# Performance work log

Measured on AMD Instinct MI355X. Metric: run time of the kernel, lower is better.

## Reference

```python
import jax, jax.numpy as jnp
import numpy as np

N_EMBED = 1024
HEAD_SIZE = 64
SEQ_LEN = 4096
BATCH = 4


def setup_inputs() -> dict:
    key = jax.random.key(0)
    ks = jax.random.split(key, 7)
    scale = 1.0 / np.sqrt(N_EMBED)
    return {
        "x": jax.random.normal(ks[0], (BATCH, SEQ_LEN, N_EMBED), dtype=jnp.float32),
        "Wq": jax.random.normal(ks[1], (N_EMBED, HEAD_SIZE), dtype=jnp.float32) * scale,
        "bq": jax.random.normal(ks[2], (HEAD_SIZE,), dtype=jnp.float32) * 0.01,
        "Wk": jax.random.normal(ks[3], (N_EMBED, HEAD_SIZE), dtype=jnp.float32) * scale,
        "bk": jax.random.normal(ks[4], (HEAD_SIZE,), dtype=jnp.float32) * 0.01,
        "Wv": jax.random.normal(ks[5], (N_EMBED, HEAD_SIZE), dtype=jnp.float32) * scale,
        "bv": jax.random.normal(ks[6], (HEAD_SIZE,), dtype=jnp.float32) * 0.01,
    }


def reference(x, Wq, bq, Wk, bk, Wv, bv):
    # q, k, v: [B, S, H]
    q = x @ Wq + bq
    k = x @ Wk + bk
    v = x @ Wv + bv
    # raw scores [B, S, S]; original masks to -inf THEN divides by sqrt(head_size)
    # (-inf / sqrt = -inf, so equivalent to scaling finite entries only)
    scores = jnp.einsum("bqh,bkh->bqk", q, k)
    seq_len = x.shape[1]
    causal = jnp.tril(jnp.ones((seq_len, seq_len), dtype=bool))
    inv_scale = 1.0 / jnp.sqrt(jnp.asarray(HEAD_SIZE, dtype=scores.dtype))
    scores = jnp.where(causal, scores * inv_scale, -jnp.inf)
    weight = jax.nn.softmax(scores, axis=-1)
    # dropout is identity in eval / p=0
    out = jnp.einsum("bqk,bkh->bqh", weight, v)
    return out
```

## Files before the change

kernel.cpp:

```cpp
#include <hip/hip_runtime.h>
#include <hip/hip_bf16.h>

#define SS 4096
#define NROW 16384

typedef __attribute__((ext_vector_type(8))) short short8;
typedef __attribute__((ext_vector_type(4))) short short4_t;
typedef __attribute__((ext_vector_type(4))) float f32x4;

static __device__ __forceinline__ short f2bf(float f) {
    union { float f; unsigned u; } v; v.f = f;
    unsigned r = v.u + 0x7FFFu + ((v.u >> 16) & 1u);
    return (short)(r >> 16);
}
static __device__ __forceinline__ float bf2f(short s) {
    union { unsigned u; float f; } v;
    v.u = ((unsigned)(unsigned short)s) << 16;
    return v.f;
}

__global__ __launch_bounds__(256) void pack_w(const float* __restrict__ Wq,
                                              const float* __restrict__ Wk,
                                              const float* __restrict__ Wv,
                                              short* __restrict__ Wpack) {
    int t = blockIdx.x * 256 + threadIdx.x;
    int n = t % 192;
    int k = t / 192;
    const float* W = (n < 64) ? Wq : (n < 128 ? Wk : Wv);
    int nn = n & 63;
    Wpack[n * 1024 + k] = f2bf(W[k * 64 + nn]);
}

__global__ __launch_bounds__(256, 2) void proj_qkv(const float* __restrict__ x,
                                                   const short* __restrict__ Wpack,
                                                   const float* __restrict__ bq,
                                                   const float* __restrict__ bk,
                                                   const float* __restrict__ bv,
                                                   short* __restrict__ Qg,
                                                   short* __restrict__ Kg,
                                                   short* __restrict__ Vt) {
    __shared__ short Xs[2][32 * 72];
    __shared__ short Wsm[2][192 * 72];
    int tid = threadIdx.x, lane = tid & 63, wv = tid >> 6;
    int g = lane >> 4, c = lane & 15;
    int mh = wv & 1, nh = wv >> 1;
    int rowbase = blockIdx.x * 32;

    f32x4 acc[6];
    for (int i = 0; i < 6; ++i) acc[i] = (f32x4)(0.f);

    int xrow0 = tid >> 4, xc = tid & 15;
    const float* xp0 = x + (rowbase + xrow0) * 1024 + xc * 4;
    const float* xp1 = x + (rowbase + 16 + xrow0) * 1024 + xc * 4;

    float4 xr0 = *reinterpret_cast<const float4*>(xp0);
    float4 xr1 = *reinterpret_cast<const float4*>(xp1);
    short8 wr[6];
    for (int j = 0; j < 6; ++j) {
        int u = tid + j * 256;
        wr[j] = *reinterpret_cast<const short8*>(Wpack + (u >> 3) * 1024 + (u & 7) * 8);
    }

    for (int ko = 0; ko < 16; ++ko) {
        int bs = ko & 1;
        short4_t s0, s1;
        s0.x = f2bf(xr0.x); s0.y = f2bf(xr0.y); s0.z = f2bf(xr0.z); s0.w = f2bf(xr0.w);
        s1.x = f2bf(xr1.x); s1.y = f2bf(xr1.y); s1.z = f2bf(xr1.z); s1.w = f2bf(xr1.w);
        *reinterpret_cast<short4_t*>(&Xs[bs][xrow0 * 72 + xc * 4]) = s0;
        *reinterpret_cast<short4_t*>(&Xs[bs][(16 + xrow0) * 72 + xc * 4]) = s1;
        for (int j = 0; j < 6; ++j) {
            int u = tid + j * 256;
            *reinterpret_cast<short8*>(&Wsm[bs][(u >> 3) * 72 + (u & 7) * 8]) = wr[j];
        }
        if (ko < 15) {
            int k0 = (ko + 1) * 64;
            xr0 = *reinterpret_cast<const float4*>(xp0 + k0);
            xr1 = *reinterpret_cast<const float4*>(xp1 + k0);
            for (int j = 0; j < 6; ++j) {
                int u = tid + j * 256;
                wr[j] = *reinterpret_cast<const short8*>(Wpack + (u >> 3) * 1024 + k0 + (u & 7) * 8);
            }
        }
        __syncthreads();
        for (int kc = 0; kc < 2; ++kc) {
            short8 a = *reinterpret_cast<const short8*>(&Xs[bs][(mh * 16 + c) * 72 + kc * 32 + g * 8]);
            for (int nt = 0; nt < 6; ++nt) {
                short8 b = *reinterpret_cast<const short8*>(&Wsm[bs][(nh * 96 + nt * 16 + c) * 72 + kc * 32 + g * 8]);
                acc[nt] = __builtin_amdgcn_mfma_f32_16x16x32_bf16(a, b, acc[nt], 0, 0, 0);
            }
        }
    }

    const float SCQ = 0.125f * 1.4426950408889634f;
    for (int nt = 0; nt < 6; ++nt) {
        int col = nh * 96 + nt * 16 + c;
        for (int r = 0; r < 4; ++r) {
            int grow = rowbase + mh * 16 + g * 4 + r;
            float vv = acc[nt][r];
            if (col < 64) {
                Qg[grow * 64 + col] = f2bf((vv + bq[col]) * SCQ);
            } else if (col < 128) {
                Kg[grow * 64 + (col - 64)] = f2bf(vv + bk[col - 64]);
            } else {
                int f = col - 128;
                int batch = grow >> 12, s = grow & 4095;
                Vt[batch * 262144 + (s >> 6) * 4096 + f * 64 + (s & 63)] = f2bf(vv + bv[f]);
            }
        }
    }
}

__global__ __launch_bounds__(256, 3) void attn(const short* __restrict__ Qg,
                                               const short* __restrict__ Kg,
                                               const short* __restrict__ Vt,
                                               short* __restrict__ Opart,
                                               float* __restrict__ Ls) {
    __shared__ short Kbuf[2][64 * 72];
    __shared__ short Vbuf[2][64 * 72];
    __shared__ short Ps[4][16 * 68];
    int tid = threadIdx.x, lane = tid & 63, wv = tid >> 6;
    int g = lane >> 4, c = lane & 15;

    int b = blockIdx.x;
    int ch = b & 7, P = (b >> 3) & 63, batch = b >> 9;
    int ntall = P + 1;
    int nch = (ntall + 7) >> 3;
    if (ch >= nch) return;
    int t0 = ch * 8, t1 = min(t0 + 8, ntall);

    int qrow0 = batch * SS + P * 64;
    const short* Kb = Kg + batch * SS * 64;
    const short* Vb = Vt + batch * SS * 64;

    short8 aq0 = *reinterpret_cast<const short8*>(Qg + (qrow0 + wv * 16 + c) * 64 + g * 8);
    short8 aq1 = *reinterpret_cast<const short8*>(Qg + (qrow0 + wv * 16 + c) * 64 + 32 + g * 8);

    f32x4 acc_o[4];
    for (int f = 0; f < 4; ++f) acc_o[f] = (f32x4)(0.f);
    float rs[4] = {0.f, 0.f, 0.f, 0.f};

    int u0 = tid, u1 = tid + 256;
    short8 kr0 = *reinterpret_cast<const short8*>(Kb + t0 * 4096 + u0 * 8);
    short8 kr1 = *reinterpret_cast<const short8*>(Kb + t0 * 4096 + u1 * 8);
    short8 vr0 = *reinterpret_cast<const short8*>(Vb + t0 * 4096 + u0 * 8);
    short8 vr1 = *reinterpret_cast<const short8*>(Vb + t0 * 4096 + u1 * 8);

    short* Psw = Ps[wv];

    for (int t = t0; t < t1; ++t) {
        int bs = t & 1;
        *reinterpret_cast<short8*>(&Kbuf[bs][(u0 >> 3) * 72 + (u0 & 7) * 8]) = kr0;
        *reinterpret_cast<short8*>(&Kbuf[bs][(u1 >> 3) * 72 + (u1 & 7) * 8]) = kr1;
        *reinterpret_cast<short8*>(&Vbuf[bs][(u0 >> 3) * 72 + (u0 & 7) * 8]) = vr0;
        *reinterpret_cast<short8*>(&Vbuf[bs][(u1 >> 3) * 72 + (u1 & 7) * 8]) = vr1;
        if (t + 1 < t1) {
            kr0 = *reinterpret_cast<const short8*>(Kb + (t + 1) * 4096 + u0 * 8);
            kr1 = *reinterpret_cast<const short8*>(Kb + (t + 1) * 4096 + u1 * 8);
            vr0 = *reinterpret_cast<const short8*>(Vb + (t + 1) * 4096 + u0 * 8);
            vr1 = *reinterpret_cast<const short8*>(Vb + (t + 1) * 4096 + u1 * 8);
        }
        __syncthreads();

        f32x4 s[4];
        for (int nt = 0; nt < 4; ++nt) s[nt] = (f32x4)(0.f);
        for (int nt = 0; nt < 4; ++nt) {
            short8 b0 = *reinterpret_cast<const short8*>(&Kbuf[bs][(nt * 16 + c) * 72 + g * 8]);
            s[nt] = __builtin_amdgcn_mfma_f32_16x16x32_bf16(aq0, b0, s[nt], 0, 0, 0);
            short8 b1 = *reinterpret_cast<const short8*>(&Kbuf[bs][(nt * 16 + c) * 72 + 32 + g * 8]);
            s[nt] = __builtin_amdgcn_mfma_f32_16x16x32_bf16(aq1, b1, s[nt], 0, 0, 0);
        }

        if (t == P) {
            for (int nt = 0; nt < 4; ++nt)
                for (int r = 0; r < 4; ++r) {
                    int key = nt * 16 + c;
                    int row = wv * 16 + g * 4 + r;
                    float p = (key <= row) ? exp2f(s[nt][r]) : 0.f;
                    rs[r] += p;
                    Psw[(g * 4 + r) * 68 + nt * 16 + c] = f2bf(p);
                }
        } else {
            for (int nt = 0; nt < 4; ++nt)
                for (int r = 0; r < 4; ++r) {
                    float p = exp2f(s[nt][r]);
                    rs[r] += p;
                    Psw[(g * 4 + r) * 68 + nt * 16 + c] = f2bf(p);
                }
        }

        for (int kc2 = 0; kc2 < 2; ++kc2) {
            short8 ap = *reinterpret_cast<const short8*>(&Psw[c * 68 + kc2 * 32 + g * 8]);
            for (int f = 0; f < 4; ++f) {
                short8 bv_ = *reinterpret_cast<const short8*>(&Vbuf[bs][(f * 16 + c) * 72 + kc2 * 32 + g * 8]);
                acc_o[f] = __builtin_amdgcn_mfma_f32_16x16x32_bf16(ap, bv_, acc_o[f], 0, 0, 0);
            }
        }
    }

    float l[4];
    for (int r = 0; r < 4; ++r) {
        float ss = rs[r];
        ss += __shfl_xor(ss, 1);
        ss += __shfl_xor(ss, 2);
        ss += __shfl_xor(ss, 4);
        ss += __shfl_xor(ss, 8);
        l[r] = ss;
    }

    int slot = ((batch * 64 + P) << 3) + ch;
    short* op = Opart + slot * 4096;
    for (int r = 0; r < 4; ++r) {
        float inv = 1.0f / l[r];
        int row = wv * 16 + g * 4 + r;
        for (int f = 0; f < 4; ++f)
            op[row * 64 + f * 16 + c] = f2bf(acc_o[f][r] * inv);
    }
    if (c == 0)
        for (int r = 0; r < 4; ++r)
            Ls[slot * 64 + wv * 16 + g * 4 + r] = l[r];
}

__global__ __launch_bounds__(256) void merge_k(const short* __restrict__ Opart,
                                               const float* __restrict__ Ls,
                                               float* __restrict__ out) {
    int bP = blockIdx.x;
    int P = bP & 63, batch = bP >> 6;
    int nch = (P + 8) >> 3;
    int tid = threadIdx.x;
    int row = tid & 63, fg = tid >> 6;
    int slot0 = bP << 3;

    float w[8];
    float wsum = 0.f;
    for (int i = 0; i < nch; ++i) { w[i] = Ls[(slot0 + i) * 64 + row]; wsum += w[i]; }
    float invw = 1.0f / wsum;

    float o[16];
    for (int j = 0; j < 16; ++j) o[j] = 0.f;
    for (int i = 0; i < nch; ++i) {
        const short* op = Opart + (slot0 + i) * 4096 + row * 64 + fg * 16;
        short8 v0 = *reinterpret_cast<const short8*>(op);
        short8 v1 = *reinterpret_cast<const short8*>(op + 8);
        for (int j = 0; j < 8; ++j) {
            o[j]     += w[i] * bf2f(v0[j]);
            o[8 + j] += w[i] * bf2f(v1[j]);
        }
    }
    int orow = batch * SS + P * 64 + row;
    for (int j = 0; j < 16; j += 4) {
        float4 v;
        v.x = o[j] * invw; v.y = o[j + 1] * invw; v.z = o[j + 2] * invw; v.w = o[j + 3] * invw;
        *reinterpret_cast<float4*>(out + orow * 64 + fg * 16 + j) = v;
    }
}

extern "C" void kernel_launch(void* const* d_in, const int* in_sizes, int n_in,
                              void* d_out, int out_size, void* d_ws, size_t ws_size,
                              hipStream_t stream) {
    const float* x  = (const float*)d_in[0];
    const float* Wq = (const float*)d_in[1];
    const float* bq = (const float*)d_in[2];
    const float* Wk = (const float*)d_in[3];
    const float* bk = (const float*)d_in[4];
    const float* Wv = (const float*)d_in[5];
    const float* bv = (const float*)d_in[6];
    float* out = (float*)d_out;

    short* Wpack = (short*)d_ws;
    short* Qg    = Wpack + 196608;
    short* Kg    = Qg + NROW * 64;
    short* Vt    = Kg + NROW * 64;
    short* Opart = Vt + NROW * 64;
    float* Ls    = (float*)(Opart + 2048 * 4096);

    hipLaunchKernelGGL(pack_w,   dim3(768),  dim3(256), 0, stream, Wq, Wk, Wv, Wpack);
    hipLaunchKernelGGL(proj_qkv, dim3(512),  dim3(256), 0, stream, x, Wpack, bq, bk, bv, Qg, Kg, Vt);
    hipLaunchKernelGGL(attn,     dim3(2048), dim3(256), 0, stream, Qg, Kg, Vt, Opart, Ls);
    hipLaunchKernelGGL(merge_k,  dim3(256),  dim3(256), 0, stream, Opart, Ls, out);
}
```

Before: 178.8 us.

## Use direct global-to-LDS loads with XOR swizzle, compact attention grid, faster bf16/exp

Replaces register-staged global loads in the projection and attention kernels with global_load_lds transfers into XOR-swizzled, unpadded LDS tiles. x is now kept as fp32 in LDS and converted to bf16 at fragment-read time. The attention grid is remapped so that only valid (query tile, chunk) pairs are launched, which removes the empty blocks that previously returned early. It also switches to the hardware exp2 and a cheaper round-to-nearest bf16 conversion, and rewrites pack_w as an LDS-tiled transpose. The risks are subtle swizzle and index bugs, a slightly different rounding mode, and larger fp32 LDS usage.

```diff
diff --git a/kernel.cpp b/kernel.cpp
--- a/kernel.cpp
+++ b/kernel.cpp
@@ -5,14 +5,27 @@
 #define NROW 16384
 
 typedef __attribute__((ext_vector_type(8))) short short8;
-typedef __attribute__((ext_vector_type(4))) short short4_t;
 typedef __attribute__((ext_vector_type(4))) float f32x4;
 
+#define AS1 __attribute__((address_space(1)))
+#define AS3 __attribute__((address_space(3)))
+
+static __device__ __forceinline__ void glds16(const void* g, void* l) {
+    __builtin_amdgcn_global_load_lds((const AS1 unsigned*)g, (AS3 unsigned*)l, 16, 0, 0);
+}
 static __device__ __forceinline__ short f2bf(float f) {
     union { float f; unsigned u; } v; v.f = f;
     unsigned r = v.u + 0x7FFFu + ((v.u >> 16) & 1u);
     return (short)(r >> 16);
 }
+static __device__ __forceinline__ short f2bf_fast(float f) {
+    union { float f; unsigned u; } v; v.f = f;
+    return (short)((v.u + 0x8000u) >> 16);
+}
+static __device__ __forceinline__ unsigned pkbf(float lo, float hi) {
+    union { float f; unsigned u; } x, y; x.f = lo; y.f = hi;
+    return __builtin_amdgcn_perm(y.u + 0x8000u, x.u + 0x8000u, 0x07060302);
+}
 static __device__ __forceinline__ float bf2f(short s) {
     union { unsigned u; float f; } v;
     v.u = ((unsigned)(unsigned short)s) << 16;
@@ -23,12 +36,23 @@
                                               const float* __restrict__ Wk,
                                               const float* __restrict__ Wv,
                                               short* __restrict__ Wpack) {
-    int t = blockIdx.x * 256 + threadIdx.x;
-    int n = t % 192;
-    int k = t / 192;
-    const float* W = (n < 64) ? Wq : (n < 128 ? Wk : Wv);
-    int nn = n & 63;
-    Wpack[n * 1024 + k] = f2bf(W[k * 64 + nn]);
+    __shared__ float T[64 * 65];
+    int bid = blockIdx.x;
+    int nb = bid >> 4, kb = bid & 15;
+    const float* W = (nb == 0) ? Wq : (nb == 1 ? Wk : Wv);
+    int n0 = nb * 64, k0 = kb * 64;
+    int tid = threadIdx.x;
+    for (int ps = 0; ps < 16; ++ps) {
+        int idx = tid + ps * 256;
+        int kk = idx >> 6, nn = idx & 63;
+        T[kk * 65 + nn] = W[(k0 + kk) * 64 + nn];
+    }
+    __syncthreads();
+    for (int ps = 0; ps < 16; ++ps) {
+        int idx = tid + ps * 256;
+        int nn = idx >> 6, kk = idx & 63;
+        Wpack[(n0 + nn) * 1024 + k0 + kk] = f2bf(T[kk * 65 + nn]);
+    }
 }
 
 __global__ __launch_bounds__(256, 2) void proj_qkv(const float* __restrict__ x,
@@ -39,8 +63,8 @@
                                                    short* __restrict__ Qg,
                                                    short* __restrict__ Kg,
                                                    short* __restrict__ Vt) {
-    __shared__ short Xs[2][32 * 72];
-    __shared__ short Wsm[2][192 * 72];
+    __shared__ float Xs[2][32 * 64];
+    __shared__ short Wsm[2][192 * 64];
     int tid = threadIdx.x, lane = tid & 63, wv = tid >> 6;
     int g = lane >> 4, c = lane & 15;
     int mh = wv & 1, nh = wv >> 1;
@@ -49,47 +73,43 @@
     f32x4 acc[6];
     for (int i = 0; i < 6; ++i) acc[i] = (f32x4)(0.f);
 
-    int xrow0 = tid >> 4, xc = tid & 15;
-    const float* xp0 = x + (rowbase + xrow0) * 1024 + xc * 4;
-    const float* xp1 = x + (rowbase + 16 + xrow0) * 1024 + xc * 4;
-
-    float4 xr0 = *reinterpret_cast<const float4*>(xp0);
-    float4 xr1 = *reinterpret_cast<const float4*>(xp1);
-    short8 wr[6];
-    for (int j = 0; j < 6; ++j) {
-        int u = tid + j * 256;
-        wr[j] = *reinterpret_cast<const short8*>(Wpack + (u >> 3) * 1024 + (u & 7) * 8);
-    }
+    int xs0 = (wv * 2 + 0) * 64 + lane, xs1 = (wv * 2 + 1) * 64 + lane;
+    int xr0 = xs0 >> 4, xp0 = (xs0 & 15) ^ (xr0 & 15);
+    int xr1 = xs1 >> 4, xp1 = (xs1 & 15) ^ (xr1 & 15);
+
+#define PROJ_ISSUE(nbs, k0)                                                              \
+    do {                                                                                 \
+        glds16(x + (rowbase + xr0) * 1024 + (k0) + xp0 * 4, &Xs[nbs][(wv * 2 + 0) * 256]); \
+        glds16(x + (rowbase + xr1) * 1024 + (k0) + xp1 * 4, &Xs[nbs][(wv * 2 + 1) * 256]); \
+        for (int j = 0; j < 6; ++j) {                                                    \
+            int ws = (wv * 6 + j) * 64 + lane;                                           \
+            int wr = ws >> 3, wp = (ws & 7) ^ (wr & 7);                                  \
+            glds16(Wpack + wr * 1024 + (k0) + wp * 8, &Wsm[nbs][(wv * 6 + j) * 512]);    \
+        }                                                                                \
+    } while (0)
+
+    PROJ_ISSUE(0, 0);
 
     for (int ko = 0; ko < 16; ++ko) {
         int bs = ko & 1;
-        short4_t s0, s1;
-        s0.x = f2bf(xr0.x); s0.y = f2bf(xr0.y); s0.z = f2bf(xr0.z); s0.w = f2bf(xr0.w);
-        s1.x = f2bf(xr1.x); s1.y = f2bf(xr1.y); s1.z = f2bf(xr1.z); s1.w = f2bf(xr1.w);
-        *reinterpret_cast<short4_t*>(&Xs[bs][xrow0 * 72 + xc * 4]) = s0;
-        *reinterpret_cast<short4_t*>(&Xs[bs][(16 + xrow0) * 72 + xc * 4]) = s1;
-        for (int j = 0; j < 6; ++j) {
-            int u = tid + j * 256;
-            *reinterpret_cast<short8*>(&Wsm[bs][(u >> 3) * 72 + (u & 7) * 8]) = wr[j];
-        }
-        if (ko < 15) {
-            int k0 = (ko + 1) * 64;
-            xr0 = *reinterpret_cast<const float4*>(xp0 + k0);
-            xr1 = *reinterpret_cast<const float4*>(xp1 + k0);
-            for (int j = 0; j < 6; ++j) {
-                int u = tid + j * 256;
-                wr[j] = *reinterpret_cast<const short8*>(Wpack + (u >> 3) * 1024 + k0 + (u & 7) * 8);
-            }
-        }
         __syncthreads();
+        if (ko < 15) PROJ_ISSUE(bs ^ 1, (ko + 1) * 64);
         for (int kc = 0; kc < 2; ++kc) {
-            short8 a = *reinterpret_cast<const short8*>(&Xs[bs][(mh * 16 + c) * 72 + kc * 32 + g * 8]);
+            int h0 = kc * 8 + g * 2;
+            float4 xa = *reinterpret_cast<const float4*>(&Xs[bs][(mh * 16 + c) * 64 + ((h0) ^ c) * 4]);
+            float4 xb = *reinterpret_cast<const float4*>(&Xs[bs][(mh * 16 + c) * 64 + ((h0 + 1) ^ c) * 4]);
+            short8 a;
+            unsigned* aw = (unsigned*)&a;
+            aw[0] = pkbf(xa.x, xa.y); aw[1] = pkbf(xa.z, xa.w);
+            aw[2] = pkbf(xb.x, xb.y); aw[3] = pkbf(xb.z, xb.w);
             for (int nt = 0; nt < 6; ++nt) {
-                short8 b = *reinterpret_cast<const short8*>(&Wsm[bs][(nh * 96 + nt * 16 + c) * 72 + kc * 32 + g * 8]);
+                int wrow = nh * 96 + nt * 16 + c;
+                short8 b = *reinterpret_cast<const short8*>(&Wsm[bs][wrow * 64 + ((g + 4 * kc) ^ (c & 7)) * 8]);
                 acc[nt] = __builtin_amdgcn_mfma_f32_16x16x32_bf16(a, b, acc[nt], 0, 0, 0);
             }
         }
     }
+#undef PROJ_ISSUE
 
     const float SCQ = 0.125f * 1.4426950408889634f;
     for (int nt = 0; nt < 6; ++nt) {
@@ -115,20 +135,26 @@
                                                const short* __restrict__ Vt,
                                                short* __restrict__ Opart,
                                                float* __restrict__ Ls) {
-    __shared__ short Kbuf[2][64 * 72];
-    __shared__ short Vbuf[2][64 * 72];
+    __shared__ short Kbuf[2][64 * 64];
+    __shared__ short Vbuf[2][64 * 64];
     __shared__ short Ps[4][16 * 68];
     int tid = threadIdx.x, lane = tid & 63, wv = tid >> 6;
     int g = lane >> 4, c = lane & 15;
 
-    int b = blockIdx.x;
-    int ch = b & 7, P = (b >> 3) & 63, batch = b >> 9;
-    int ntall = P + 1;
-    int nch = (ntall + 7) >> 3;
-    if (ch >= nch) return;
+    int bid = blockIdx.x;
+    int batch = bid / 288;
+    int j = bid - batch * 288;
+    int gq = (int)((sqrtf((float)j + 1.0f) - 1.0f) * 0.5f);
+    while (4 * (gq + 1) * (gq + 2) <= j) ++gq;
+    while (4 * gq * (gq + 1) > j) --gq;
+    int rem = j - 4 * gq * (gq + 1);
+    int pidx = rem / (gq + 1);
+    int ch = rem - pidx * (gq + 1);
+    int p = gq * 8 + pidx;
+
+    int ntall = p + 1;
     int t0 = ch * 8, t1 = min(t0 + 8, ntall);
-
-    int qrow0 = batch * SS + P * 64;
+    int qrow0 = batch * SS + p * 64;
     const short* Kb = Kg + batch * SS * 64;
     const short* Vb = Vt + batch * SS * 64;
 
@@ -139,63 +165,64 @@
     for (int f = 0; f < 4; ++f) acc_o[f] = (f32x4)(0.f);
     float rs[4] = {0.f, 0.f, 0.f, 0.f};
 
-    int u0 = tid, u1 = tid + 256;
-    short8 kr0 = *reinterpret_cast<const short8*>(Kb + t0 * 4096 + u0 * 8);
-    short8 kr1 = *reinterpret_cast<const short8*>(Kb + t0 * 4096 + u1 * 8);
-    short8 vr0 = *reinterpret_cast<const short8*>(Vb + t0 * 4096 + u0 * 8);
-    short8 vr1 = *reinterpret_cast<const short8*>(Vb + t0 * 4096 + u1 * 8);
-
+    int s0 = (wv * 2 + 0) * 64 + lane, s1 = (wv * 2 + 1) * 64 + lane;
+    int r0 = s0 >> 3, q0 = ((s0 & 7) ^ (r0 & 7));
+    int r1 = s1 >> 3, q1 = ((s1 & 7) ^ (r1 & 7));
+
+#define ATTN_ISSUE(nbs, t)                                                           \
+    do {                                                                             \
+        const short* kt_ = Kb + (t) * 4096;                                          \
+        const short* vt_ = Vb + (t) * 4096;                                          \
+        glds16(kt_ + r0 * 64 + q0 * 8, &Kbuf[nbs][(wv * 2 + 0) * 512]);              \
+        glds16(kt_ + r1 * 64 + q1 * 8, &Kbuf[nbs][(wv * 2 + 1) * 512]);              \
+        glds16(vt_ + r0 * 64 + q0 * 8, &Vbuf[nbs][(wv * 2 + 0) * 512]);              \
+        glds16(vt_ + r1 * 64 + q1 * 8, &Vbuf[nbs][(wv * 2 + 1) * 512]);              \
+    } while (0)
+
+    ATTN_ISSUE(0, t0);
     short* Psw = Ps[wv];
 
     for (int t = t0; t < t1; ++t) {
-        int bs = t & 1;
-        *reinterpret_cast<short8*>(&Kbuf[bs][(u0 >> 3) * 72 + (u0 & 7) * 8]) = kr0;
-        *reinterpret_cast<short8*>(&Kbuf[bs][(u1 >> 3) * 72 + (u1 & 7) * 8]) = kr1;
-        *reinterpret_cast<short8*>(&Vbuf[bs][(u0 >> 3) * 72 + (u0 & 7) * 8]) = vr0;
-        *reinterpret_cast<short8*>(&Vbuf[bs][(u1 >> 3) * 72 + (u1 & 7) * 8]) = vr1;
-        if (t + 1 < t1) {
-            kr0 = *reinterpret_cast<const short8*>(Kb + (t + 1) * 4096 + u0 * 8);
-            kr1 = *reinterpret_cast<const short8*>(Kb + (t + 1) * 4096 + u1 * 8);
-            vr0 = *reinterpret_cast<const short8*>(Vb + (t + 1) * 4096 + u0 * 8);
-            vr1 = *reinterpret_cast<const short8*>(Vb + (t + 1) * 4096 + u1 * 8);
-        }
+        int bs = (t - t0) & 1;
         __syncthreads();
+        if (t + 1 < t1) ATTN_ISSUE(bs ^ 1, t + 1);
 
         f32x4 s[4];
         for (int nt = 0; nt < 4; ++nt) s[nt] = (f32x4)(0.f);
         for (int nt = 0; nt < 4; ++nt) {
-            short8 b0 = *reinterpret_cast<const short8*>(&Kbuf[bs][(nt * 16 + c) * 72 + g * 8]);
+            short8 b0 = *reinterpret_cast<const short8*>(&Kbuf[bs][(nt * 16 + c) * 64 + ((g) ^ (c & 7)) * 8]);
             s[nt] = __builtin_amdgcn_mfma_f32_16x16x32_bf16(aq0, b0, s[nt], 0, 0, 0);
-            short8 b1 = *reinterpret_cast<const short8*>(&Kbuf[bs][(nt * 16 + c) * 72 + 32 + g * 8]);
+            short8 b1 = *reinterpret_cast<const short8*>(&Kbuf[bs][(nt * 16 + c) * 64 + ((g + 4) ^ (c & 7)) * 8]);
             s[nt] = __builtin_amdgcn_mfma_f32_16x16x32_bf16(aq1, b1, s[nt], 0, 0, 0);
         }
 
-        if (t == P) {
+        if (t == p) {
             for (int nt = 0; nt < 4; ++nt)
                 for (int r = 0; r < 4; ++r) {
                     int key = nt * 16 + c;
                     int row = wv * 16 + g * 4 + r;
-                    float p = (key <= row) ? exp2f(s[nt][r]) : 0.f;
-                    rs[r] += p;
-                    Psw[(g * 4 + r) * 68 + nt * 16 + c] = f2bf(p);
+                    float pv = (key <= row) ? __builtin_amdgcn_exp2f(s[nt][r]) : 0.f;
+                    rs[r] += pv;
+                    Psw[(g * 4 + r) * 68 + nt * 16 + c] = f2bf_fast(pv);
                 }
         } else {
             for (int nt = 0; nt < 4; ++nt)
                 for (int r = 0; r < 4; ++r) {
-                    float p = exp2f(s[nt][r]);
-                    rs[r] += p;
-                    Psw[(g * 4 + r) * 68 + nt * 16 + c] = f2bf(p);
+                    float pv = __builtin_amdgcn_exp2f(s[nt][r]);
+                    rs[r] += pv;
+                    Psw[(g * 4 + r) * 68 + nt * 16 + c] = f2bf_fast(pv);
                 }
         }
 
         for (int kc2 = 0; kc2 < 2; ++kc2) {
             short8 ap = *reinterpret_cast<const short8*>(&Psw[c * 68 + kc2 * 32 + g * 8]);
             for (int f = 0; f < 4; ++f) {
-                short8 bv_ = *reinterpret_cast<const short8*>(&Vbuf[bs][(f * 16 + c) * 72 + kc2 * 32 + g * 8]);
+                short8 bv_ = *reinterpret_cast<const short8*>(&Vbuf[bs][(f * 16 + c) * 64 + ((g + 4 * kc2) ^ (c & 7)) * 8]);
                 acc_o[f] = __builtin_amdgcn_mfma_f32_16x16x32_bf16(ap, bv_, acc_o[f], 0, 0, 0);
             }
         }
     }
+#undef ATTN_ISSUE
 
     float l[4];
     for (int r = 0; r < 4; ++r) {
@@ -207,7 +234,7 @@
         l[r] = ss;
     }
 
-    int slot = ((batch * 64 + P) << 3) + ch;
+    int slot = ((batch * 64 + p) << 3) + ch;
     short* op = Opart + slot * 4096;
     for (int r = 0; r < 4; ++r) {
         float inv = 1.0f / l[r];
@@ -236,21 +263,21 @@
     float invw = 1.0f / wsum;
 
     float o[16];
-    for (int j = 0; j < 16; ++j) o[j] = 0.f;
+    for (int jj = 0; jj < 16; ++jj) o[jj] = 0.f;
     for (int i = 0; i < nch; ++i) {
         const short* op = Opart + (slot0 + i) * 4096 + row * 64 + fg * 16;
         short8 v0 = *reinterpret_cast<const short8*>(op);
         short8 v1 = *reinterpret_cast<const short8*>(op + 8);
-        for (int j = 0; j < 8; ++j) {
-            o[j]     += w[i] * bf2f(v0[j]);
-            o[8 + j] += w[i] * bf2f(v1[j]);
+        for (int jj = 0; jj < 8; ++jj) {
+            o[jj]     += w[i] * bf2f(v0[jj]);
+            o[8 + jj] += w[i] * bf2f(v1[jj]);
         }
     }
     int orow = batch * SS + P * 64 + row;
-    for (int j = 0; j < 16; j += 4) {
+    for (int jj = 0; jj < 16; jj += 4) {
         float4 v;
-        v.x = o[j] * invw; v.y = o[j + 1] * invw; v.z = o[j + 2] * invw; v.w = o[j + 3] * invw;
-        *reinterpret_cast<float4*>(out + orow * 64 + fg * 16 + j) = v;
+        v.x = o[jj] * invw; v.y = o[jj + 1] * invw; v.z = o[jj + 2] * invw; v.w = o[jj + 3] * invw;
+        *reinterpret_cast<float4*>(out + orow * 64 + fg * 16 + jj) = v;
     }
 }
 
@@ -273,8 +300,8 @@
     short* Opart = Vt + NROW * 64;
     float* Ls    = (float*)(Opart + 2048 * 4096);
 
-    hipLaunchKernelGGL(pack_w,   dim3(768),  dim3(256), 0, stream, Wq, Wk, Wv, Wpack);
+    hipLaunchKernelGGL(pack_w,   dim3(48),   dim3(256), 0, stream, Wq, Wk, Wv, Wpack);
     hipLaunchKernelGGL(proj_qkv, dim3(512),  dim3(256), 0, stream, x, Wpack, bq, bk, bv, Qg, Kg, Vt);
-    hipLaunchKernelGGL(attn,     dim3(2048), dim3(256), 0, stream, Qg, Kg, Vt, Opart, Ls);
+    hipLaunchKernelGGL(attn,     dim3(1152), dim3(256), 0, stream, Qg, Kg, Vt, Opart, Ls);
     hipLaunchKernelGGL(merge_k,  dim3(256),  dim3(256), 0, stream, Opart, Ls, out);
 }
```

New measurement: 163.1 us. -8.8%, faster.
